# Performance work log

Measured on AMD Instinct MI355X. Metric: run time of the kernel, lower is better.

The kernel has to match this reference:

```python
import jax, jax.numpy as jnp
import numpy as np

B, N = 64, 1024

def setup_inputs() -> dict:
    key = jax.random.key(0)
    ks = jax.random.split(key, 8)
    x = jax.random.normal(ks[0], (B, N, 3), dtype=jnp.float32)
    adj = jax.random.uniform(ks[1], (B, N, N), dtype=jnp.float32)
    # Linear params stored as [in, out]; torch Linear init scale ~1/sqrt(in)
    W1 = jax.random.normal(ks[2], (3, 10), dtype=jnp.float32) / np.sqrt(3.0)
    b1 = jax.random.normal(ks[3], (10,), dtype=jnp.float32) * 0.1
    W2 = jax.random.normal(ks[4], (10, 10), dtype=jnp.float32) / np.sqrt(10.0)
    b2 = jax.random.normal(ks[5], (10,), dtype=jnp.float32) * 0.1
    W3 = jax.random.normal(ks[6], (10, 2), dtype=jnp.float32) / np.sqrt(10.0)
    b3 = jax.random.normal(ks[7], (2,), dtype=jnp.float32) * 0.1
    return {"x": x, "adj": adj, "W1": W1, "b1": b1, "W2": W2, "b2": b2, "W3": W3, "b3": b3}

def reference(x, adj, W1, b1, W2, b2, W3, b3):
    # round 1: message MLP then dense aggregation
    m1 = jnp.tanh(x @ W1 + b1)              # [B, N, 10]
    h = jnp.einsum('bnm,bmd->bnd', adj, m1) # [B, N, 10]
    # round 2
    m2 = jnp.tanh(h @ W2 + b2)              # [B, N, 10]
    h = jnp.einsum('bnm,bmd->bnd', adj, m2) # [B, N, 10]
    # sum pooling over nodes + readout
    pooled = h.sum(axis=1)                  # [B, 10]
    return pooled @ W3 + b3                 # [B, 2]
```

## Files before the change

kernel.cpp:

```cpp
#include <hip/hip_runtime.h>


typedef __attribute__((ext_vector_type(8))) short short8;
typedef __attribute__((ext_vector_type(4))) float f32x4;

__device__ __forceinline__ unsigned short f2bf(float f) {
    unsigned int u = __float_as_uint(f);
    u += 0x7FFFu + ((u >> 16) & 1u);
    return (unsigned short)(u >> 16);
}

__global__ __launch_bounds__(256) void k_mlp1(const float* __restrict__ x,
                                              const float* __restrict__ W1,
                                              const float* __restrict__ b1,
                                              unsigned short* __restrict__ bpack) {
    int g = blockIdx.x * 256 + threadIdx.x;
    int slot = g & 63;
    int b_kc = g >> 6;
    int d = slot & 15, q = slot >> 4;
    int kc = b_kc & 31, b = b_kc >> 5;
    int m0 = kc * 32 + q * 8;
    const float* xp = x + (size_t)(b * 1024 + m0) * 3;
    float w0 = 0.f, w1 = 0.f, w2 = 0.f, bb = 0.f;
    if (d < 10) { w0 = W1[d]; w1 = W1[10 + d]; w2 = W1[20 + d]; bb = b1[d]; }
    unsigned int o[8];
#pragma unroll
    for (int j = 0; j < 8; ++j) {
        float v = 0.f;
        if (d < 10) v = tanhf(xp[j*3] * w0 + xp[j*3+1] * w1 + xp[j*3+2] * w2 + bb);
        o[j] = f2bf(v);
    }
    uint4 pk;
    pk.x = o[0] | (o[1] << 16);
    pk.y = o[2] | (o[3] << 16);
    pk.z = o[4] | (o[5] << 16);
    pk.w = o[6] | (o[7] << 16);
    *(uint4*)(bpack + (size_t)g * 8) = pk;
}

__device__ __forceinline__ void cvt_store(const float4* a, unsigned short* aTb,
                                          float* csbb, int rgrp, int c32,
                                          int w, int l) {
    float cs0 = 0.f, cs1 = 0.f, cs2 = 0.f, cs3 = 0.f;
#pragma unroll
    for (int i = 0; i < 8; ++i) {
        int row = i * 8 + rgrp;
        cs0 += a[i].x; cs1 += a[i].y; cs2 += a[i].z; cs3 += a[i].w;
        unsigned int lo = f2bf(a[i].x) | ((unsigned)f2bf(a[i].y) << 16);
        unsigned int hi = f2bf(a[i].z) | ((unsigned)f2bf(a[i].w) << 16);
        unsigned bo = (unsigned)(row * 256 + c32 * 8);
        bo ^= (unsigned)((row & 7) << 4);
        *(uint2*)((char*)aTb + bo) = make_uint2(lo, hi);
    }
    cs0 += __shfl_xor(cs0, 32); cs1 += __shfl_xor(cs1, 32);
    cs2 += __shfl_xor(cs2, 32); cs3 += __shfl_xor(cs3, 32);
    if (l < 32)
        *(float4*)&csbb[w * 128 + l * 4] = make_float4(cs0, cs1, cs2, cs3);
}

__global__ __launch_bounds__(256) void k_agg(const float* __restrict__ adj,
                                             const unsigned short* __restrict__ bpack,
                                             float* __restrict__ h_ws,
                                             float* __restrict__ cs_part) {
    __shared__ __align__(16) unsigned short aT[2][64 * 128];
    __shared__ float csb[2][4 * 128];

    const int t = threadIdx.x;
    const int b = blockIdx.x >> 4;
    const int tile = blockIdx.x & 15;
    const int n0 = tile * 64;
    const int l = t & 63, w = t >> 6;
    const int rgrp = t >> 5;
    const int c32 = t & 31;

    const float* adj_base = adj + (size_t)(b * 1024 + n0) * 1024;
    const short8* bfrag = (const short8*)(bpack + (size_t)b * 16384);

    {
        float4 a0[8];
#pragma unroll
        for (int i = 0; i < 8; ++i)
            a0[i] = *(const float4*)(adj_base + (size_t)(i * 8 + rgrp) * 1024 + c32 * 4);
        cvt_store(a0, aT[0], csb[0], rgrp, c32, w, l);
    }
    __syncthreads();

    f32x4 acc = {0.f, 0.f, 0.f, 0.f};
    int p = 0;
    const int lrow = w * 16 + (l & 15);
    const int lcol0 = (l >> 4) * 16;

    for (int k = 0; k < 8; ++k) {
        float4 nx[8];
        if (k < 7) {
#pragma unroll
            for (int i = 0; i < 8; ++i)
                nx[i] = *(const float4*)(adj_base
                    + (size_t)(i * 8 + rgrp) * 1024 + (k + 1) * 128 + c32 * 4);
        }
#pragma unroll
        for (int kc = 0; kc < 4; ++kc) {
            unsigned bo = (unsigned)(lrow * 256 + kc * 64 + lcol0);
            bo ^= (unsigned)((lrow & 7) << 4);
            short8 af = *(const short8*)((char*)aT[p] + bo);
            short8 bf = bfrag[(k * 4 + kc) * 64 + l];
            acc = __builtin_amdgcn_mfma_f32_16x16x32_bf16(af, bf, acc, 0, 0, 0);
        }
        if (t < 128) {
            float s = csb[p][t] + csb[p][128 + t] + csb[p][256 + t] + csb[p][384 + t];
            cs_part[(((size_t)b * 16 + tile) * 8 + k) * 128 + t] = s;
        }
        if (k < 7) {
            cvt_store(nx, aT[p ^ 1], csb[p ^ 1], rgrp, c32, w, l);
            __syncthreads();
            p ^= 1;
        }
    }
    {
        int col = l & 15, rb = (l >> 4) * 4;
#pragma unroll
        for (int r = 0; r < 4; ++r) {
            int n = n0 + w * 16 + rb + r;
            h_ws[((size_t)(b * 1024 + n) << 4) + col] = acc[r];
        }
    }
}

__global__ __launch_bounds__(256) void k_read(const float* __restrict__ h_ws,
                                              const float* __restrict__ cs_part,
                                              const float* __restrict__ W2,
                                              const float* __restrict__ b2,
                                              const float* __restrict__ W3,
                                              const float* __restrict__ b3,
                                              float* __restrict__ out) {
    int b = blockIdx.x, t = threadIdx.x;
    float pool[10];
#pragma unroll
    for (int d = 0; d < 10; ++d) pool[d] = 0.f;

    for (int it = 0; it < 4; ++it) {
        int m = it * 256 + t;
        float cs = 0.f;
#pragma unroll
        for (int tile = 0; tile < 16; ++tile)
            cs += cs_part[(((size_t)b * 16 + tile) * 8 + (m >> 7)) * 128 + (m & 127)];
        const float* hp = h_ws + ((size_t)(b * 1024 + m) << 4);
        float hv[10];
#pragma unroll
        for (int d = 0; d < 10; ++d) hv[d] = hp[d];
#pragma unroll
        for (int dp = 0; dp < 10; ++dp) {
            float s = b2[dp];
#pragma unroll
            for (int d = 0; d < 10; ++d) s += hv[d] * W2[d * 10 + dp];
            pool[dp] += cs * tanhf(s);
        }
    }
#pragma unroll
    for (int d = 0; d < 10; ++d) {
        float v = pool[d];
        v += __shfl_xor(v, 1);  v += __shfl_xor(v, 2);  v += __shfl_xor(v, 4);
        v += __shfl_xor(v, 8);  v += __shfl_xor(v, 16); v += __shfl_xor(v, 32);
        pool[d] = v;
    }
    __shared__ float red[4][10];
    int l = t & 63, w = t >> 6;
    if (l == 0) {
#pragma unroll
        for (int d = 0; d < 10; ++d) red[w][d] = pool[d];
    }
    __syncthreads();
    if (t < 2) {
        float s = b3[t];
#pragma unroll
        for (int dp = 0; dp < 10; ++dp) {
            float p = red[0][dp] + red[1][dp] + red[2][dp] + red[3][dp];
            s += p * W3[dp * 2 + t];
        }
        out[b * 2 + t] = s;
    }
}

extern "C" void kernel_launch(void* const* d_in, const int* in_sizes, int n_in,
                              void* d_out, int out_size, void* d_ws, size_t ws_size,
                              hipStream_t stream) {
    (void)in_sizes; (void)n_in; (void)out_size; (void)ws_size;
    const float* x   = (const float*)d_in[0];
    const float* adj = (const float*)d_in[1];
    const float* W1  = (const float*)d_in[2];
    const float* b1  = (const float*)d_in[3];
    const float* W2  = (const float*)d_in[4];
    const float* b2  = (const float*)d_in[5];
    const float* W3  = (const float*)d_in[6];
    const float* b3  = (const float*)d_in[7];
    float* out = (float*)d_out;

    char* ws = (char*)d_ws;
    unsigned short* bpack = (unsigned short*)ws;
    float* h_ws    = (float*)(ws + (2u << 20));
    float* cs_part = (float*)(ws + (6u << 20));

    k_mlp1<<<512, 256, 0, stream>>>(x, W1, b1, bpack);
    k_agg<<<1024, 256, 0, stream>>>(adj, bpack, h_ws, cs_part);
    k_read<<<64, 256, 0, stream>>>(h_ws, cs_part, W2, b2, W3, b3, out);
}
```

Baseline: 383.3 us.

## Deepen adj prefetch to two stages and fuse W2 MLP into aggregation epilogue

The aggregation kernel now prefetches adjacency chunks two iterations ahead using alternating register buffers in a fully unrolled macro loop. It also preloads the B fragments one step early. The second message MLP (h@W2+b2, tanh) moves into the k_agg epilogue through shared memory, so the readout kernel only does the weighted pooling. This aims to hide more HBM latency in the bandwidth-bound adj stream and to spread the MLP work across 1024 blocks instead of 64, at the cost of higher register pressure.

Measured after the change: 373.6 us (median of 2 runs). -2.5%, faster.

```diff
diff --git a/kernel.cpp b/kernel.cpp
--- a/kernel.cpp
+++ b/kernel.cpp
@@ -60,8 +60,10 @@
 
 __global__ __launch_bounds__(256) void k_agg(const float* __restrict__ adj,
                                              const unsigned short* __restrict__ bpack,
-                                             float* __restrict__ h_ws,
-                                             float* __restrict__ cs_part) {
+                                             float* __restrict__ m2c,
+                                             float* __restrict__ cs_part,
+                                             const float* __restrict__ W2,
+                                             const float* __restrict__ b2) {
     __shared__ __align__(16) unsigned short aT[2][64 * 128];
     __shared__ float csb[2][4 * 128];
 
@@ -76,60 +78,89 @@
     const float* adj_base = adj + (size_t)(b * 1024 + n0) * 1024;
     const short8* bfrag = (const short8*)(bpack + (size_t)b * 16384);
 
-    {
-        float4 a0[8];
-#pragma unroll
-        for (int i = 0; i < 8; ++i)
-            a0[i] = *(const float4*)(adj_base + (size_t)(i * 8 + rgrp) * 1024 + c32 * 4);
-        cvt_store(a0, aT[0], csb[0], rgrp, c32, w, l);
-    }
+    float4 nxA[8], nxB[8];
+    short8 bfb[4];
+
+#pragma unroll
+    for (int i = 0; i < 8; ++i)
+        nxA[i] = *(const float4*)(adj_base + (size_t)(i * 8 + rgrp) * 1024 + c32 * 4);
+#pragma unroll
+    for (int i = 0; i < 8; ++i)
+        nxB[i] = *(const float4*)(adj_base + (size_t)(i * 8 + rgrp) * 1024 + 128 + c32 * 4);
+#pragma unroll
+    for (int kc = 0; kc < 4; ++kc) bfb[kc] = bfrag[kc * 64 + l];
+    cvt_store(nxA, aT[0], csb[0], rgrp, c32, w, l);
     __syncthreads();
 
     f32x4 acc = {0.f, 0.f, 0.f, 0.f};
-    int p = 0;
     const int lrow = w * 16 + (l & 15);
     const int lcol0 = (l >> 4) * 16;
 
-    for (int k = 0; k < 8; ++k) {
-        float4 nx[8];
-        if (k < 7) {
-#pragma unroll
-            for (int i = 0; i < 8; ++i)
-                nx[i] = *(const float4*)(adj_base
-                    + (size_t)(i * 8 + rgrp) * 1024 + (k + 1) * 128 + c32 * 4);
-        }
-#pragma unroll
-        for (int kc = 0; kc < 4; ++kc) {
-            unsigned bo = (unsigned)(lrow * 256 + kc * 64 + lcol0);
-            bo ^= (unsigned)((lrow & 7) << 4);
-            short8 af = *(const short8*)((char*)aT[p] + bo);
-            short8 bf = bfrag[(k * 4 + kc) * 64 + l];
-            acc = __builtin_amdgcn_mfma_f32_16x16x32_bf16(af, bf, acc, 0, 0, 0);
-        }
-        if (t < 128) {
-            float s = csb[p][t] + csb[p][128 + t] + csb[p][256 + t] + csb[p][384 + t];
-            cs_part[(((size_t)b * 16 + tile) * 8 + k) * 128 + t] = s;
-        }
-        if (k < 7) {
-            cvt_store(nx, aT[p ^ 1], csb[p ^ 1], rgrp, c32, w, l);
-            __syncthreads();
-            p ^= 1;
-        }
-    }
+#define K_ITER(K, NXLOAD, NXSTORE)                                             \
+    {                                                                          \
+        if ((K) < 6) {                                                         \
+            _Pragma("unroll")                                                  \
+            for (int i = 0; i < 8; ++i)                                        \
+                NXLOAD[i] = *(const float4*)(adj_base                          \
+                    + (size_t)(i * 8 + rgrp) * 1024 + ((K) + 2) * 128 + c32 * 4); \
+        }                                                                      \
+        _Pragma("unroll")                                                      \
+        for (int kc = 0; kc < 4; ++kc) {                                       \
+            unsigned bo = (unsigned)(lrow * 256 + kc * 64 + lcol0);            \
+            bo ^= (unsigned)((lrow & 7) << 4);                                 \
+            short8 af = *(const short8*)((char*)aT[(K) & 1] + bo);             \
+            acc = __builtin_amdgcn_mfma_f32_16x16x32_bf16(af, bfb[kc], acc, 0, 0, 0); \
+        }                                                                      \
+        if ((K) < 7) {                                                         \
+            _Pragma("unroll")                                                  \
+            for (int kc = 0; kc < 4; ++kc)                                     \
+                bfb[kc] = bfrag[(((K) + 1) * 4 + kc) * 64 + l];                \
+        }                                                                      \
+        if (t < 128) {                                                         \
+            float s = csb[(K) & 1][t] + csb[(K) & 1][128 + t]                  \
+                    + csb[(K) & 1][256 + t] + csb[(K) & 1][384 + t];           \
+            cs_part[(((size_t)b * 16 + tile) * 8 + (K)) * 128 + t] = s;        \
+        }                                                                      \
+        if ((K) < 7) {                                                         \
+            cvt_store(NXSTORE, aT[((K) + 1) & 1], csb[((K) + 1) & 1],          \
+                      rgrp, c32, w, l);                                        \
+            __syncthreads();                                                   \
+        }                                                                      \
+    }
+
+    K_ITER(0, nxA, nxB)
+    K_ITER(1, nxB, nxA)
+    K_ITER(2, nxA, nxB)
+    K_ITER(3, nxB, nxA)
+    K_ITER(4, nxA, nxB)
+    K_ITER(5, nxB, nxA)
+    K_ITER(6, nxA, nxB)
+    K_ITER(7, nxB, nxA)
+#undef K_ITER
+
+    float* hbuf = (float*)aT;
     {
         int col = l & 15, rb = (l >> 4) * 4;
 #pragma unroll
-        for (int r = 0; r < 4; ++r) {
-            int n = n0 + w * 16 + rb + r;
-            h_ws[((size_t)(b * 1024 + n) << 4) + col] = acc[r];
+        for (int r = 0; r < 4; ++r)
+            hbuf[(w * 16 + rb + r) * 16 + col] = acc[r];
+    }
+    __syncthreads();
+#pragma unroll
+    for (int j = 0; j < 4; ++j) {
+        int slot = t + j * 256;
+        int node = slot >> 4, dp = slot & 15;
+        if (dp < 10) {
+            float s = b2[dp];
+#pragma unroll
+            for (int d = 0; d < 10; ++d) s += hbuf[node * 16 + d] * W2[d * 10 + dp];
+            m2c[((size_t)(b * 1024 + n0 + node) << 4) + dp] = tanhf(s);
         }
     }
 }
 
-__global__ __launch_bounds__(256) void k_read(const float* __restrict__ h_ws,
+__global__ __launch_bounds__(256) void k_read(const float* __restrict__ m2c,
                                               const float* __restrict__ cs_part,
-                                              const float* __restrict__ W2,
-                                              const float* __restrict__ b2,
                                               const float* __restrict__ W3,
                                               const float* __restrict__ b3,
                                               float* __restrict__ out) {
@@ -144,17 +175,15 @@
 #pragma unroll
         for (int tile = 0; tile < 16; ++tile)
             cs += cs_part[(((size_t)b * 16 + tile) * 8 + (m >> 7)) * 128 + (m & 127)];
-        const float* hp = h_ws + ((size_t)(b * 1024 + m) << 4);
-        float hv[10];
-#pragma unroll
-        for (int d = 0; d < 10; ++d) hv[d] = hp[d];
-#pragma unroll
-        for (int dp = 0; dp < 10; ++dp) {
-            float s = b2[dp];
-#pragma unroll
-            for (int d = 0; d < 10; ++d) s += hv[d] * W2[d * 10 + dp];
-            pool[dp] += cs * tanhf(s);
-        }
+        const float* mp = m2c + ((size_t)(b * 1024 + m) << 4);
+        float4 v0 = *(const float4*)mp;
+        float4 v1 = *(const float4*)(mp + 4);
+        float2 v2 = *(const float2*)(mp + 8);
+        pool[0] += cs * v0.x; pool[1] += cs * v0.y;
+        pool[2] += cs * v0.z; pool[3] += cs * v0.w;
+        pool[4] += cs * v1.x; pool[5] += cs * v1.y;
+        pool[6] += cs * v1.z; pool[7] += cs * v1.w;
+        pool[8] += cs * v2.x; pool[9] += cs * v2.y;
     }
 #pragma unroll
     for (int d = 0; d < 10; ++d) {
@@ -197,10 +226,10 @@
 
     char* ws = (char*)d_ws;
     unsigned short* bpack = (unsigned short*)ws;
-    float* h_ws    = (float*)(ws + (2u << 20));
+    float* m2c     = (float*)(ws + (2u << 20));
     float* cs_part = (float*)(ws + (6u << 20));
 
     k_mlp1<<<512, 256, 0, stream>>>(x, W1, b1, bpack);
-    k_agg<<<1024, 256, 0, stream>>>(adj, bpack, h_ws, cs_part);
-    k_read<<<64, 256, 0, stream>>>(h_ws, cs_part, W2, b2, W3, b3, out);
-}
+    k_agg<<<1024, 256, 0, stream>>>(adj, bpack, m2c, cs_part, W2, b2);
+    k_read<<<64, 256, 0, stream>>>(m2c, cs_part, W3, b3, out);
+}
```
